# Performance work log

Measured on AMD Instinct MI355X. Metric: run time of the kernel, lower is better.

The kernel has to match this reference:

```python
import jax, jax.numpy as jnp
import numpy as np

PC = 512      # proposal_channels == conv_channels
INCH = 512    # in_channels of branch
B = 8
T = 64        # pyramid level length (feat_t) at order=0
TF = 256      # frame_level_feature length (clip_length)
KERNELS = [8, 16, 8, 4, 2, 2, 2]  # ConPoolingKernal
CLC = 498     # feature_lastclass channels (CLC + 2 == 500)
GROUPS = 32


def _gn(x, gamma, beta):
    # GroupNorm(32, C) over [B, C, L]
    Bb, C, L = x.shape
    xg = x.reshape(Bb, GROUPS, C // GROUPS, L)
    m = xg.mean(axis=(2, 3), keepdims=True)
    v = xg.var(axis=(2, 3), keepdims=True)
    xn = ((xg - m) * jax.lax.rsqrt(v + 1e-5)).reshape(Bb, C, L)
    return xn * gamma[None, :, None] + beta[None, :, None]


def _c1(x, w, b):
    # Unit1D kernel_shape=1: pointwise conv
    return jnp.einsum('bct,oc->bot', x, w) + b[None, :, None]


def _bmp(feat, segs):
    # BoundaryMaxPooling: first C/2 channels max-pooled over segs[...,0:2],
    # second C/2 over segs[...,2:4] (inclusive integer ranges, clamped).
    Bb, C, L = feat.shape
    C2 = C // 2
    pos = jnp.arange(L)
    def pool(f, s, e):
        s = jnp.clip(s, 0, L - 1)
        e = jnp.maximum(jnp.clip(e, 0, L - 1), s)
        mask = (pos[None, None, :] >= s[..., None]) & (pos[None, None, :] <= e[..., None])  # [B,T,L]
        return jnp.max(jnp.where(mask[:, None], f[:, :, None, :], -jnp.inf), axis=-1)  # [B,C2,T]
    return jnp.concatenate([pool(feat[:, :C2], segs[..., 0], segs[..., 1]),
                            pool(feat[:, C2:], segs[..., 2], segs[..., 3])], axis=1)


def _anchor_gather(feat, anc, K):
    # Vectorized per-anchor clamp/slice + nearest F.interpolate(size=K):
    # src index for output k of a slice [l, r] is l + floor(k * (r - l + 1) / K).
    Bb, C, L = feat.shape
    left = jnp.clip(anc[..., 0], 0, L)
    right = jnp.clip(anc[..., 1], 0, L)
    valid = right > left                      # empty slices -> zeros (torch branch)
    seglen = right + 1 - left
    k = jnp.arange(K)
    idx = jnp.clip(left[..., None] + (k[None, None, :] * seglen[..., None]) // K, 0, L - 1)  # [B,T,K]
    g = jax.vmap(lambda f, ix: f[:, ix])(feat, idx)   # [B,C,T,K]
    return g * valid[:, None, :, None].astype(feat.dtype)


def setup_inputs() -> dict:
    key = jax.random.key(0)
    ks = jax.random.split(key, 16)
    f32 = jnp.float32
    s = 0.02
    def w(k, shape):
        return jax.random.normal(k, shape, f32) * s
    inp = {}
    inp['feature'] = jax.random.normal(ks[0], (B, INCH, T), f32)
    inp['frame_level_feature'] = jax.random.normal(ks[1], (B, PC, TF), f32)
    inp['segments'] = jax.random.randint(ks[2], (B, T, 4), 0, T).astype(jnp.int32)
    inp['frame_segments'] = jax.random.randint(ks[3], (B, T, 4), 0, TF).astype(jnp.int32)
    inp['feature_lastclass'] = jax.random.normal(ks[4], (B, CLC, T), f32)
    inp['anchor'] = jnp.sort(jax.random.randint(ks[5], (B, T, 2), 0, T), axis=-1).astype(jnp.int32)
    inp['frame_anchor'] = jnp.sort(jax.random.randint(ks[6], (B, T, 2), 0, TF), axis=-1).astype(jnp.int32)
    inp['order'] = 0
    inp['LocResult_feature'] = jax.random.normal(ks[7], (B, 2, T), f32)
    inp['w_cur'] = w(ks[8], (PC, INCH)); inp['b_cur'] = jnp.zeros((PC,), f32)
    inp['g_cur'] = jnp.ones((PC,), f32); inp['be_cur'] = jnp.zeros((PC,), f32)
    inp['w_lr'] = w(ks[9], (2 * PC, INCH)); inp['b_lr'] = jnp.zeros((2 * PC,), f32)
    inp['g_lr'] = jnp.ones((2 * PC,), f32); inp['be_lr'] = jnp.zeros((2 * PC,), f32)
    inp['w_roi'] = w(ks[10], (PC, PC)); inp['b_roi'] = jnp.zeros((PC,), f32)
    inp['g_roi'] = jnp.ones((PC,), f32); inp['be_roi'] = jnp.zeros((PC,), f32)
    K1 = KERNELS[1]; K0 = KERNELS[0]
    inp['w_cp'] = w(ks[11], (PC, 2 * PC, K1)); inp['b_cp'] = jnp.zeros((PC,), f32)
    inp['w_cp0'] = w(ks[12], (PC, PC, K0)); inp['b_cp0'] = jnp.zeros((PC,), f32)
    CIN = 6 * PC + 500
    inp['w_prop'] = w(ks[13], (INCH, CIN)); inp['b_prop'] = jnp.zeros((INCH,), f32)
    inp['g_prop'] = jnp.ones((INCH,), f32); inp['be_prop'] = jnp.zeros((INCH,), f32)
    return inp


def reference(feature, frame_level_feature, segments, frame_segments, feature_lastclass,
              anchor, frame_anchor, order, LocResult_feature,
              w_cur, b_cur, g_cur, be_cur, w_lr, b_lr, g_lr, be_lr,
              w_roi, b_roi, g_roi, be_roi, w_cp, b_cp, w_cp0, b_cp0,
              w_prop, b_prop, g_prop, be_prop):
    relu = jax.nn.relu
    fm_short = relu(_gn(_c1(feature, w_cur, b_cur), g_cur, be_cur))           # [B,PC,T]
    feat_lr = relu(_gn(_c1(feature, w_lr, b_lr), g_lr, be_lr))                # [B,2PC,T]
    prop_feature = _bmp(feat_lr, segments)                                    # [B,2PC,T]
    prop_roi = relu(_gn(_c1(_bmp(frame_level_feature, frame_segments), w_roi, b_roi), g_roi, be_roi))
    K1 = KERNELS[order + 1]
    K0 = KERNELS[0]
    g1 = _anchor_gather(feat_lr, anchor, K1)                                  # [B,2PC,T,K1]
    con_feature = jnp.einsum('bctk,ock->bot', g1, w_cp) + b_cp[None, :, None]  # valid conv K1->1
    g0 = _anchor_gather(frame_level_feature, frame_anchor, K0)                # [B,PC,T,K0]
    frame_con = jnp.einsum('bctk,ock->bot', g0, w_cp0) + b_cp0[None, :, None]
    prop_con = relu(_gn(_c1(frame_con, w_roi, b_roi), g_roi, be_roi))
    cat = jnp.concatenate([prop_roi, prop_feature, fm_short, feature_lastclass,
                           con_feature, prop_con, LocResult_feature], axis=1)  # [B,6PC+500,T]
    out = relu(_gn(_c1(cat, w_prop, b_prop), g_prop, be_prop))                # [B,INCH,T]
    return (out, feat_lr)
```

## Files before the change

kernel.cpp:

```cpp
#include <hip/hip_runtime.h>
#include <math.h>

#define BB 8
#define CATP 3584
#define CAT_REAL 3572

typedef __attribute__((ext_vector_type(8))) short short8;
typedef __attribute__((ext_vector_type(4))) float f32x4;

__device__ inline ushort f2bf(float f) {
  union { float f; unsigned u; } x;
  x.f = f;
  return (ushort)((x.u + 0x7FFFu + ((x.u >> 16) & 1u)) >> 16);
}
__device__ inline float bf2f(unsigned us) {
  union { unsigned u; float f; } x;
  x.u = us << 16;
  return x.f;
}

__global__ __launch_bounds__(256) void cvt_wfrag_kernel(
    const float* __restrict__ w_cur, const float* __restrict__ w_lr,
    const float* __restrict__ w_roi, const float* __restrict__ w_prop,
    ushort* __restrict__ Wcomb, ushort* __restrict__ Wroi,
    ushort* __restrict__ Wprop) {
  const int i = blockIdx.x * 256 + threadIdx.x;
  const float* src;
  ushort* dst;
  int o, k8, Kc;
  bool pad = false;
  if (i < 98304) {
    o = i >> 6; k8 = i & 63; Kc = 16;
    src = (o < 512) ? (w_cur + (size_t)o * 512) : (w_lr + (size_t)(o - 512) * 512);
    dst = Wcomb;
  } else if (i < 131072) {
    const int r = i - 98304;
    o = r >> 6; k8 = r & 63; Kc = 16;
    src = w_roi + (size_t)o * 512;
    dst = Wroi;
  } else {
    const int r = i - 131072;
    if (r >= 229376) return;
    o = r / 448; k8 = r % 448; Kc = 112;
    src = w_prop + (size_t)o * CAT_REAL;
    dst = Wprop;
    pad = true;
  }
  const int k = k8 * 8;
  float v[8];
  if (pad) {
#pragma unroll
    for (int q = 0; q < 8; q++) v[q] = (k + q < CAT_REAL) ? src[k + q] : 0.f;
  } else {
    const float4 f0 = *(const float4*)(src + k);
    const float4 f1 = *(const float4*)(src + k + 4);
    v[0] = f0.x; v[1] = f0.y; v[2] = f0.z; v[3] = f0.w;
    v[4] = f1.x; v[5] = f1.y; v[6] = f1.z; v[7] = f1.w;
  }
  uint4 pk;
  pk.x = (unsigned)f2bf(v[0]) | ((unsigned)f2bf(v[1]) << 16);
  pk.y = (unsigned)f2bf(v[2]) | ((unsigned)f2bf(v[3]) << 16);
  pk.z = (unsigned)f2bf(v[4]) | ((unsigned)f2bf(v[5]) << 16);
  pk.w = (unsigned)f2bf(v[6]) | ((unsigned)f2bf(v[7]) << 16);
  const int ot = o >> 6, ii = (o >> 4) & 3, l15 = o & 15;
  const int kc = k8 >> 2, l4 = k8 & 3;
  const size_t flat =
      ((((size_t)ot * Kc + kc) * 4 + ii) * 64 + l4 * 16 + l15) * 8;
  *(uint4*)(dst + flat) = pk;
}

template <int Cin, int Kf>
__device__ void cpT_body(const float* __restrict__ W, ushort* __restrict__ D,
                         int o, float* tile ) {
  const int nt = o >> 6, j = (o >> 4) & 3, l15 = o & 15;
  for (int c0 = 0; c0 < Cin; c0 += 256) {
    __syncthreads();
    for (int e = threadIdx.x; e < 256 * Kf; e += 256) {
      const int c = e / Kf, k = e % Kf;
      tile[c * (Kf + 1) + k] = W[((size_t)o * Cin + c0) * Kf + e];
    }
    __syncthreads();
    for (int e = threadIdx.x; e < Kf * 32; e += 256) {
      const int k = e >> 5, c8 = e & 31;
      const int cl = c8 * 8;
      const int c = c0 + cl;
      uint4 pk;
      pk.x = (unsigned)f2bf(tile[(cl + 0) * (Kf + 1) + k]) |
             ((unsigned)f2bf(tile[(cl + 1) * (Kf + 1) + k]) << 16);
      pk.y = (unsigned)f2bf(tile[(cl + 2) * (Kf + 1) + k]) |
             ((unsigned)f2bf(tile[(cl + 3) * (Kf + 1) + k]) << 16);
      pk.z = (unsigned)f2bf(tile[(cl + 4) * (Kf + 1) + k]) |
             ((unsigned)f2bf(tile[(cl + 5) * (Kf + 1) + k]) << 16);
      pk.w = (unsigned)f2bf(tile[(cl + 6) * (Kf + 1) + k]) |
             ((unsigned)f2bf(tile[(cl + 7) * (Kf + 1) + k]) << 16);
      const int cc = c >> 5, l4 = (c >> 3) & 3;
      const size_t flat =
          ((((size_t)nt * Kf + k) * (Cin >> 5) + cc) * 4 + j) * 512 +
          (l4 * 16 + l15) * 8;
      *(uint4*)(D + flat) = pk;
    }
  }
}

__global__ __launch_bounds__(256) void cvt_cpT_kernel(
    const float* __restrict__ w_cp, ushort* __restrict__ WcpT,
    const float* __restrict__ w_cp0, ushort* __restrict__ Wcp0T) {
  __shared__ float tile[256 * 17];
  const int bid = blockIdx.x;
  if (bid < 512)
    cpT_body<1024, 16>(w_cp, WcpT, bid, tile);
  else
    cpT_body<512, 8>(w_cp0, Wcp0T, bid - 512, tile);
}

__global__ __launch_bounds__(256) void transpose_multi_kernel(
    const float* __restrict__ feature, const float* __restrict__ frame_feat,
    const float* __restrict__ lastcls, const float* __restrict__ locres,
    ushort* __restrict__ Ft, ushort* __restrict__ FfT,
    ushort* __restrict__ cat) {
  const int bid = blockIdx.x;
  const float* src;
  ushort* dst;
  int Cr, Cw, L, rs, co, cblk, lblk, b;
  if (bid < 64) {
    src = feature; dst = Ft; Cr = 512; Cw = 512; L = 64; rs = 512; co = 0;
    cblk = bid & 7; lblk = 0; b = bid >> 3;
  } else if (bid < 320) {
    const int r = bid - 64;
    src = frame_feat; dst = FfT; Cr = 512; Cw = 512; L = 256; rs = 512; co = 0;
    cblk = r & 7; lblk = (r >> 3) & 3; b = r >> 5;
  } else if (bid < 384) {
    const int r = bid - 320;
    src = lastcls; dst = cat; Cr = 498; Cw = 498; L = 64; rs = CATP; co = 2048;
    cblk = r & 7; lblk = 0; b = r >> 3;
  } else {
    const int r = bid - 384;
    src = locres; dst = cat; Cr = 2; Cw = 14; L = 64; rs = CATP; co = 3570;
    cblk = 0; lblk = 0; b = r;
  }
  __shared__ float tile[64 * 65];
  const int c0 = cblk * 64, l0 = lblk * 64;
  for (int e = threadIdx.x; e < 4096; e += 256) {
    const int cc = e >> 6, ll = e & 63;
    const int c = c0 + cc;
    tile[cc * 65 + ll] = (c < Cr) ? src[((size_t)b * Cr + c) * L + l0 + ll] : 0.f;
  }
  __syncthreads();
  for (int e = threadIdx.x; e < 4096; e += 256) {
    const int ll = e >> 6, cc = e & 63;
    const int c = c0 + cc;
    if (c < Cw)
      dst[((size_t)b * L + l0 + ll) * rs + co + c] = f2bf(tile[cc * 65 + ll]);
  }
}

__global__ __launch_bounds__(256) void gemm_gn_seg_kernel(
    int nblk0,
    const ushort* __restrict__ X0, const ushort* __restrict__ W0,
    const float* __restrict__ b0, const float* __restrict__ g0,
    const float* __restrict__ e0, int Kp0, int cs0, float* of0, int om0,
    ushort* co0, int cst0, int coff0,
    const ushort* __restrict__ X1, const ushort* __restrict__ W1,
    const float* __restrict__ b1, const float* __restrict__ g1,
    const float* __restrict__ e1, int Kp1, int cs1, float* of1, int om1,
    ushort* co1, int cst1, int coff1) {
  const int bx = blockIdx.x;
  const bool s1 = bx >= nblk0;
  const ushort* Xt = s1 ? X1 : X0;
  const ushort* Wb = s1 ? W1 : W0;
  const float* bias = s1 ? b1 : b0;
  const float* gamma = s1 ? g1 : g0;
  const float* beta = s1 ? e1 : e0;
  const int Kp = s1 ? Kp1 : Kp0;
  const int cpgShift = s1 ? cs1 : cs0;
  float* outF = s1 ? of1 : of0;
  const int outFM = s1 ? om1 : om0;
  ushort* catOut = s1 ? co1 : co0;
  const int catStride = s1 ? cst1 : cst0;
  const int chOff = s1 ? coff1 : coff0;
  const int o0 = (s1 ? bx - nblk0 : bx) * 64;

  const int b = blockIdx.y;
  const int w = threadIdx.x >> 6;
  const int lane = threadIdx.x & 63;
  const int l15 = lane & 15, l4 = lane >> 4;
  const int wk = Kp >> 2;
  const int kbeg = w * wk, kend = kbeg + wk;

  f32x4 acc[4][4] = {};
  const ushort* wbase = Wb + (size_t)(o0 >> 6) * (Kp >> 5) * 2048 + lane * 8;
  const ushort* bp[4];
#pragma unroll
  for (int j = 0; j < 4; j++)
    bp[j] = Xt + (size_t)(b * 64 + j * 16 + l15) * Kp + l4 * 8;

  for (int k = kbeg; k < kend; k += 32) {
    const int kc = k >> 5;
    short8 a[4], x[4];
#pragma unroll
    for (int i = 0; i < 4; i++)
      a[i] = *(const short8*)(wbase + ((size_t)kc * 4 + i) * 512);
#pragma unroll
    for (int j = 0; j < 4; j++) x[j] = *(const short8*)(bp[j] + k);
#pragma unroll
    for (int i = 0; i < 4; i++)
#pragma unroll
      for (int j = 0; j < 4; j++)
        acc[i][j] = __builtin_amdgcn_mfma_f32_16x16x32_bf16(a[i], x[j],
                                                            acc[i][j], 0, 0, 0);
  }

  __shared__ float red[64 * 65];
  for (int ww = 0; ww < 4; ww++) {
    __syncthreads();
    if (w == ww) {
#pragma unroll
      for (int i = 0; i < 4; i++)
#pragma unroll
        for (int j = 0; j < 4; j++)
#pragma unroll
          for (int r = 0; r < 4; r++) {
            const int m = i * 16 + l4 * 4 + r;
            const int n = j * 16 + l15;
            if (ww == 0)
              red[m * 65 + n] = acc[i][j][r] + bias[o0 + m];
            else
              red[m * 65 + n] += acc[i][j][r];
          }
    }
  }
  __syncthreads();

  const int cpg = 1 << cpgShift;
  const int ngroups = 64 >> cpgShift;
  __shared__ float rs[4], rss[4], gmean[4], grstd[4];
  for (int gi = 0; gi < ngroups; gi++) {
    float s = 0.f, ss = 0.f;
    const int nel = cpg << 6;
    for (int e = threadIdx.x; e < nel; e += 256) {
      const float v = red[((gi << cpgShift) + (e >> 6)) * 65 + (e & 63)];
      s += v;
      ss += v * v;
    }
#pragma unroll
    for (int off = 32; off > 0; off >>= 1) {
      s += __shfl_down(s, off);
      ss += __shfl_down(ss, off);
    }
    if (lane == 0) { rs[w] = s; rss[w] = ss; }
    __syncthreads();
    if (threadIdx.x == 0) {
      const float ts = rs[0] + rs[1] + rs[2] + rs[3];
      const float tss = rss[0] + rss[1] + rss[2] + rss[3];
      const float mean = ts / (float)nel;
      const float var = tss / (float)nel - mean * mean;
      gmean[gi] = mean;
      grstd[gi] = rsqrtf(var + 1e-5f);
    }
    __syncthreads();
  }

  if (outF) {
    for (int e = threadIdx.x; e < 4096; e += 256) {
      const int m = e >> 6, n = e & 63;
      const int gi = m >> cpgShift;
      const int c = o0 + m;
      float v = (red[m * 65 + n] - gmean[gi]) * grstd[gi] * gamma[c] + beta[c];
      v = fmaxf(v, 0.f);
      outF[((size_t)b * outFM + c) * 64 + n] = v;
    }
  }
  if (catOut) {
    for (int e = threadIdx.x; e < 4096; e += 256) {
      const int n = e >> 6, m = e & 63;
      const int gi = m >> cpgShift;
      const int c = o0 + m;
      float v = (red[m * 65 + n] - gmean[gi]) * grstd[gi] * gamma[c] + beta[c];
      v = fmaxf(v, 0.f);
      catOut[((size_t)(b * 64) + n) * catStride + chOff + c] = f2bf(v);
    }
  }
}

template <int C, int L>
__device__ void bmp_body(const ushort* __restrict__ Xt,
                         const int* __restrict__ segs, ushort* __restrict__ Y,
                         int rowStride, int chOff, float2 (*pmax)[512]) {
  constexpr int C2 = C / 2;
  constexpr int P2 = C2 / 2;
  constexpr int CH = P2 / 64;
  const int t = blockIdx.x;
  const int b = blockIdx.y;
  const int w = threadIdx.x >> 6;
  const int lane = threadIdx.x & 63;
  const int* sg = segs + ((size_t)b * 64 + t) * 4;
  const ushort* Xb = Xt + (size_t)b * L * C;
#pragma unroll
  for (int h = 0; h < 2; h++) {
    const int s = min(max(sg[2 * h], 0), L - 1);
    const int e = max(min(max(sg[2 * h + 1], 0), L - 1), s);
#pragma unroll
    for (int q = 0; q < CH; q++) {
      const int p = q * 64 + lane;
      const ushort* base = Xb + h * C2 + 2 * p;
      float a0 = -INFINITY, a1 = -INFINITY;
      float c0 = -INFINITY, c1 = -INFINITY;
      int l = s + w;
      for (; l + 4 <= e; l += 8) {
        const unsigned u0 = *(const unsigned*)(base + (size_t)l * C);
        const unsigned u1 = *(const unsigned*)(base + (size_t)(l + 4) * C);
        a0 = fmaxf(a0, bf2f(u0 & 0xffffu));
        a1 = fmaxf(a1, bf2f(u0 >> 16));
        c0 = fmaxf(c0, bf2f(u1 & 0xffffu));
        c1 = fmaxf(c1, bf2f(u1 >> 16));
      }
      if (l <= e) {
        const unsigned u0 = *(const unsigned*)(base + (size_t)l * C);
        a0 = fmaxf(a0, bf2f(u0 & 0xffffu));
        a1 = fmaxf(a1, bf2f(u0 >> 16));
      }
      pmax[w][h * P2 + p] = make_float2(fmaxf(a0, c0), fmaxf(a1, c1));
    }
  }
  __syncthreads();
  for (int idx = threadIdx.x; idx < 2 * P2; idx += 256) {
    float2 m = pmax[0][idx];
#pragma unroll
    for (int ww = 1; ww < 4; ww++) {
      const float2 v = pmax[ww][idx];
      m.x = fmaxf(m.x, v.x);
      m.y = fmaxf(m.y, v.y);
    }
    const unsigned o = (unsigned)f2bf(m.x) | ((unsigned)f2bf(m.y) << 16);
    *(unsigned*)(Y + ((size_t)(b * 64) + t) * rowStride + chOff + 2 * idx) = o;
  }
}

__global__ __launch_bounds__(256) void bmp_dual_kernel(
    const ushort* __restrict__ FlrT, const int* __restrict__ segments,
    ushort* __restrict__ cat, const ushort* __restrict__ FfT,
    const int* __restrict__ frame_segs, ushort* __restrict__ XbmpT) {
  __shared__ float2 pm[4][512];
  if (blockIdx.z == 0)
    bmp_body<1024, 64>(FlrT, segments, cat, CATP, 512, pm);
  else
    bmp_body<512, 256>(FfT, frame_segs, XbmpT, 512, 0, pm);
}

template <int Kf, int L, int Cin>
__device__ void anchor_mfma_body(const ushort* __restrict__ src,
                                 const int* __restrict__ anc,
                                 const ushort* __restrict__ Wt,
                                 float* __restrict__ P, int slice, float* red) {
  const int nt = blockIdx.x;
  const int b = blockIdx.y;
  const int w = threadIdx.x >> 6;
  const int lane = threadIdx.x & 63;
  const int l15 = lane & 15, l4 = lane >> 4;
  const int kz = slice >> 1, chalf = slice & 1;
  const int k = kz * 4 + w;
  const int cbase = chalf * (Cin / 2);

  const ushort* rp[4];
#pragma unroll
  for (int i = 0; i < 4; i++) {
    const int t = i * 16 + l15;
    const int a0 = anc[((size_t)b * 64 + t) * 2 + 0];
    const int a1 = anc[((size_t)b * 64 + t) * 2 + 1];
    const int left = min(max(a0, 0), L);
    const int right = min(max(a1, 0), L);
    const int seglen = right + 1 - left;
    const int ix = min(max(left + (k * seglen) / Kf, 0), L - 1);
    rp[i] = src + ((size_t)b * L + ix) * Cin + cbase + l4 * 8;
  }
  const ushort* wb = Wt + (size_t)(nt * Kf + k) * (Cin >> 5) * 2048 + lane * 8;

  f32x4 acc[4][4] = {};
  for (int c0 = 0; c0 < Cin / 2; c0 += 32) {
    const int cc = (cbase + c0) >> 5;
    short8 a[4], bb[4];
#pragma unroll
    for (int i = 0; i < 4; i++) a[i] = *(const short8*)(rp[i] + c0);
#pragma unroll
    for (int j = 0; j < 4; j++)
      bb[j] = *(const short8*)(wb + ((size_t)cc * 4 + j) * 512);
#pragma unroll
    for (int i = 0; i < 4; i++)
#pragma unroll
      for (int j = 0; j < 4; j++)
        acc[i][j] = __builtin_amdgcn_mfma_f32_16x16x32_bf16(a[i], bb[j],
                                                            acc[i][j], 0, 0, 0);
  }

  for (int ww = 0; ww < 4; ww++) {
    __syncthreads();
    if (w == ww) {
#pragma unroll
      for (int i = 0; i < 4; i++)
#pragma unroll
        for (int j = 0; j < 4; j++)
#pragma unroll
          for (int r = 0; r < 4; r++) {
            const int m = i * 16 + l4 * 4 + r;
            const int n = j * 16 + l15;
            if (ww == 0)
              red[m * 65 + n] = acc[i][j][r];
            else
              red[m * 65 + n] += acc[i][j][r];
          }
    }
  }
  __syncthreads();
  float* Pp = P + (((size_t)slice * BB + b) * 512 + nt * 64) * 64;
  for (int e = threadIdx.x; e < 4096; e += 256) {
    const int n = e >> 6, m = e & 63;
    Pp[e] = red[m * 65 + n];
  }
}

__global__ __launch_bounds__(256) void anchor_mfma_dual_kernel(
    const ushort* __restrict__ FlrT, const int* __restrict__ anchor,
    const ushort* __restrict__ WcpT, float* __restrict__ P1,
    const ushort* __restrict__ FfT, const int* __restrict__ frame_anchor,
    const ushort* __restrict__ Wcp0T, float* __restrict__ P0) {
  __shared__ float red[64 * 65];
  const int z = blockIdx.z;
  if (z < 8)
    anchor_mfma_body<16, 64, 1024>(FlrT, anchor, WcpT, P1, z, red);
  else
    anchor_mfma_body<8, 256, 512>(FfT, frame_anchor, Wcp0T, P0, z - 8, red);
}

__device__ void anchor_reduce_body(const float* __restrict__ P, int ks,
                                   const float* __restrict__ bias,
                                   const int* __restrict__ anc, int L,
                                   ushort* __restrict__ Y, int rowStride,
                                   int chOff, float* tile, float* sval) {
  const int o0 = blockIdx.x * 64;
  const int b = blockIdx.y;
  if (threadIdx.x < 64) {
    const int t = threadIdx.x;
    const int a0 = anc[((size_t)b * 64 + t) * 2 + 0];
    const int a1 = anc[((size_t)b * 64 + t) * 2 + 1];
    const int left = min(max(a0, 0), L);
    const int right = min(max(a1, 0), L);
    sval[t] = (right > left) ? 1.f : 0.f;
  }
  __syncthreads();
  for (int e = threadIdx.x; e < 4096; e += 256) {
    const int nl = e >> 6, m = e & 63;
    const int n = o0 + nl;
    float s = 0.f;
    for (int z = 0; z < ks; z++)
      s += P[(((size_t)z * BB + b) * 512 + n) * 64 + m];
    tile[nl * 65 + m] = s * sval[m] + bias[n];
  }
  __syncthreads();
  for (int e = threadIdx.x; e < 4096; e += 256) {
    const int m = e >> 6, nl = e & 63;
    Y[((size_t)(b * 64) + m) * rowStride + chOff + o0 + nl] =
        f2bf(tile[nl * 65 + m]);
  }
}

__global__ __launch_bounds__(256) void anchor_reduce_dual_kernel(
    const float* __restrict__ P1, const float* __restrict__ b_cp,
    const int* __restrict__ anchor, ushort* __restrict__ cat,
    const float* __restrict__ P0, const float* __restrict__ b_cp0,
    const int* __restrict__ frame_anchor, ushort* __restrict__ FconT) {
  __shared__ float tile[64 * 65];
  __shared__ float sval[64];
  if (blockIdx.z == 0)
    anchor_reduce_body(P1, 8, b_cp, anchor, 64, cat, CATP, 2546, tile, sval);
  else
    anchor_reduce_body(P0, 4, b_cp0, frame_anchor, 256, FconT, 512, 0, tile, sval);
}

extern "C" void kernel_launch(void* const* d_in, const int* in_sizes, int n_in,
                              void* d_out, int out_size, void* d_ws,
                              size_t ws_size, hipStream_t stream) {
  const float* feature      = (const float*)d_in[0];
  const float* frame_feat   = (const float*)d_in[1];
  const int*   segments     = (const int*)d_in[2];
  const int*   frame_segs   = (const int*)d_in[3];
  const float* feat_lastcls = (const float*)d_in[4];
  const int*   anchor       = (const int*)d_in[5];
  const int*   frame_anchor = (const int*)d_in[6];
  const float* locres       = (const float*)d_in[8];
  const float* w_cur  = (const float*)d_in[9];
  const float* b_cur  = (const float*)d_in[10];
  const float* g_cur  = (const float*)d_in[11];
  const float* be_cur = (const float*)d_in[12];
  const float* w_lr   = (const float*)d_in[13];
  const float* b_lr   = (const float*)d_in[14];
  const float* g_lr   = (const float*)d_in[15];
  const float* be_lr  = (const float*)d_in[16];
  const float* w_roi  = (const float*)d_in[17];
  const float* b_roi  = (const float*)d_in[18];
  const float* g_roi  = (const float*)d_in[19];
  const float* be_roi = (const float*)d_in[20];
  const float* w_cp   = (const float*)d_in[21];
  const float* b_cp   = (const float*)d_in[22];
  const float* w_cp0  = (const float*)d_in[23];
  const float* b_cp0  = (const float*)d_in[24];
  const float* w_prop = (const float*)d_in[25];
  const float* b_prop = (const float*)d_in[26];
  const float* g_prop = (const float*)d_in[27];
  const float* be_prop= (const float*)d_in[28];

  float* out_main = (float*)d_out;
  float* feat_lr  = (float*)d_out + BB * 512 * 64;

  ushort* cat_t  = (ushort*)d_ws;
  ushort* Ft     = cat_t + 1835008;
  ushort* XbmpT  = Ft + 262144;
  ushort* FconT  = XbmpT + 262144;
  ushort* Wcomb  = FconT + 262144;
  ushort* Wroi   = Wcomb + 786432;
  ushort* Wprop  = Wroi + 262144;
  ushort* WcpT   = Wprop + 1835008;
  ushort* Wcp0T  = WcpT + 8388608;
  ushort* FlrT   = Wcp0T + 2097152;
  ushort* FfT    = FlrT + 524288;
  float*  P1     = (float*)(FfT + 1048576);
  float*  P0     = P1 + 2097152;

  cvt_wfrag_kernel<<<1408, 256, 0, stream>>>(
      w_cur, w_lr, w_roi, w_prop, Wcomb, Wroi, Wprop);

  cvt_cpT_kernel<<<1024, 256, 0, stream>>>(w_cp, WcpT, w_cp0, Wcp0T);

  transpose_multi_kernel<<<392, 256, 0, stream>>>(
      feature, frame_feat, feat_lastcls, locres, Ft, FfT, cat_t);

  gemm_gn_seg_kernel<<<dim3(24, BB), 256, 0, stream>>>(
      8,
      Ft, Wcomb, b_cur, g_cur, be_cur, 512, 4, nullptr, 0, cat_t, CATP, 1536,
      Ft, Wcomb + 512 * 512, b_lr, g_lr, be_lr, 512, 5, feat_lr, 1024, FlrT,
      1024, 0);

  bmp_dual_kernel<<<dim3(64, BB, 2), 256, 0, stream>>>(
      FlrT, segments, cat_t, FfT, frame_segs, XbmpT);

  anchor_mfma_dual_kernel<<<dim3(8, BB, 12), 256, 0, stream>>>(
      FlrT, anchor, WcpT, P1, FfT, frame_anchor, Wcp0T, P0);

  anchor_reduce_dual_kernel<<<dim3(8, BB, 2), 256, 0, stream>>>(
      P1, b_cp, anchor, cat_t, P0, b_cp0, frame_anchor, FconT);

  gemm_gn_seg_kernel<<<dim3(16, BB), 256, 0, stream>>>(
      8,
      XbmpT, Wroi, b_roi, g_roi, be_roi, 512, 4, nullptr, 0, cat_t, CATP, 0,
      FconT, Wroi, b_roi, g_roi, be_roi, 512, 4, nullptr, 0, cat_t, CATP, 3058);

  gemm_gn_seg_kernel<<<dim3(8, BB), 256, 0, stream>>>(
      8,
      cat_t, Wprop, b_prop, g_prop, be_prop, CATP, 4, out_main, 512, nullptr,
      CATP, 0,
      cat_t, Wprop, b_prop, g_prop, be_prop, CATP, 4, nullptr, 0, nullptr,
      CATP, 0);
}
```

Baseline: 308.6 us.

## Fuse prep kernels, register-transpose conv weights, split-K final GEMM with reduce

Merges the three weight/feature conversion kernels into one prep launch, which removes two launches. The conv-pool weight transpose now runs in registers with float4 loads, with no shared-memory tile or barriers. The final 3584-wide GEMM, which previously ran on only 64 blocks, is split across 4 K-chunks into fp32 partials. A separate kernel then reduces the partials and applies bias, GroupNorm and ReLU. This raises parallelism for the largest GEMM, at the cost of extra partial-buffer traffic and one more launch.

```diff
diff --git a/kernel.cpp b/kernel.cpp
--- a/kernel.cpp
+++ b/kernel.cpp
@@ -19,126 +19,126 @@
   return x.f;
 }
 
-__global__ __launch_bounds__(256) void cvt_wfrag_kernel(
+template <int Cin, int Kf>
+__device__ void cpT_tile(const float* __restrict__ W, ushort* __restrict__ D,
+                         int nt, int cc) {
+  const int tid = threadIdx.x;
+  const int j = tid >> 6, l4 = (tid >> 4) & 3, l15 = tid & 15;
+  const int o = nt * 64 + j * 16 + l15;
+  const int cb = cc * 32 + l4 * 8;
+  ushort rg[8][Kf];
+#pragma unroll
+  for (int q = 0; q < 8; q++) {
+    const float* row = W + ((size_t)o * Cin + cb + q) * Kf;
+#pragma unroll
+    for (int kq = 0; kq < Kf / 4; kq++) {
+      const float4 f = *(const float4*)(row + kq * 4);
+      rg[q][kq * 4 + 0] = f2bf(f.x);
+      rg[q][kq * 4 + 1] = f2bf(f.y);
+      rg[q][kq * 4 + 2] = f2bf(f.z);
+      rg[q][kq * 4 + 3] = f2bf(f.w);
+    }
+  }
+#pragma unroll
+  for (int k = 0; k < Kf; k++) {
+    uint4 pk;
+    pk.x = (unsigned)rg[0][k] | ((unsigned)rg[1][k] << 16);
+    pk.y = (unsigned)rg[2][k] | ((unsigned)rg[3][k] << 16);
+    pk.z = (unsigned)rg[4][k] | ((unsigned)rg[5][k] << 16);
+    pk.w = (unsigned)rg[6][k] | ((unsigned)rg[7][k] << 16);
+    *(uint4*)(D + ((size_t)(nt * Kf + k) * (Cin >> 5) + cc) * 2048 + tid * 8) = pk;
+  }
+}
+
+__global__ __launch_bounds__(256) void prep_kernel(
     const float* __restrict__ w_cur, const float* __restrict__ w_lr,
     const float* __restrict__ w_roi, const float* __restrict__ w_prop,
     ushort* __restrict__ Wcomb, ushort* __restrict__ Wroi,
-    ushort* __restrict__ Wprop) {
-  const int i = blockIdx.x * 256 + threadIdx.x;
-  const float* src;
-  ushort* dst;
-  int o, k8, Kc;
-  bool pad = false;
-  if (i < 98304) {
-    o = i >> 6; k8 = i & 63; Kc = 16;
-    src = (o < 512) ? (w_cur + (size_t)o * 512) : (w_lr + (size_t)(o - 512) * 512);
-    dst = Wcomb;
-  } else if (i < 131072) {
-    const int r = i - 98304;
-    o = r >> 6; k8 = r & 63; Kc = 16;
-    src = w_roi + (size_t)o * 512;
-    dst = Wroi;
-  } else {
-    const int r = i - 131072;
-    if (r >= 229376) return;
-    o = r / 448; k8 = r % 448; Kc = 112;
-    src = w_prop + (size_t)o * CAT_REAL;
-    dst = Wprop;
-    pad = true;
-  }
-  const int k = k8 * 8;
-  float v[8];
-  if (pad) {
-#pragma unroll
-    for (int q = 0; q < 8; q++) v[q] = (k + q < CAT_REAL) ? src[k + q] : 0.f;
-  } else {
-    const float4 f0 = *(const float4*)(src + k);
-    const float4 f1 = *(const float4*)(src + k + 4);
-    v[0] = f0.x; v[1] = f0.y; v[2] = f0.z; v[3] = f0.w;
-    v[4] = f1.x; v[5] = f1.y; v[6] = f1.z; v[7] = f1.w;
-  }
-  uint4 pk;
-  pk.x = (unsigned)f2bf(v[0]) | ((unsigned)f2bf(v[1]) << 16);
-  pk.y = (unsigned)f2bf(v[2]) | ((unsigned)f2bf(v[3]) << 16);
-  pk.z = (unsigned)f2bf(v[4]) | ((unsigned)f2bf(v[5]) << 16);
-  pk.w = (unsigned)f2bf(v[6]) | ((unsigned)f2bf(v[7]) << 16);
-  const int ot = o >> 6, ii = (o >> 4) & 3, l15 = o & 15;
-  const int kc = k8 >> 2, l4 = k8 & 3;
-  const size_t flat =
-      ((((size_t)ot * Kc + kc) * 4 + ii) * 64 + l4 * 16 + l15) * 8;
-  *(uint4*)(dst + flat) = pk;
-}
-
-template <int Cin, int Kf>
-__device__ void cpT_body(const float* __restrict__ W, ushort* __restrict__ D,
-                         int o, float* tile ) {
-  const int nt = o >> 6, j = (o >> 4) & 3, l15 = o & 15;
-  for (int c0 = 0; c0 < Cin; c0 += 256) {
-    __syncthreads();
-    for (int e = threadIdx.x; e < 256 * Kf; e += 256) {
-      const int c = e / Kf, k = e % Kf;
-      tile[c * (Kf + 1) + k] = W[((size_t)o * Cin + c0) * Kf + e];
-    }
-    __syncthreads();
-    for (int e = threadIdx.x; e < Kf * 32; e += 256) {
-      const int k = e >> 5, c8 = e & 31;
-      const int cl = c8 * 8;
-      const int c = c0 + cl;
-      uint4 pk;
-      pk.x = (unsigned)f2bf(tile[(cl + 0) * (Kf + 1) + k]) |
-             ((unsigned)f2bf(tile[(cl + 1) * (Kf + 1) + k]) << 16);
-      pk.y = (unsigned)f2bf(tile[(cl + 2) * (Kf + 1) + k]) |
-             ((unsigned)f2bf(tile[(cl + 3) * (Kf + 1) + k]) << 16);
-      pk.z = (unsigned)f2bf(tile[(cl + 4) * (Kf + 1) + k]) |
-             ((unsigned)f2bf(tile[(cl + 5) * (Kf + 1) + k]) << 16);
-      pk.w = (unsigned)f2bf(tile[(cl + 6) * (Kf + 1) + k]) |
-             ((unsigned)f2bf(tile[(cl + 7) * (Kf + 1) + k]) << 16);
-      const int cc = c >> 5, l4 = (c >> 3) & 3;
-      const size_t flat =
-          ((((size_t)nt * Kf + k) * (Cin >> 5) + cc) * 4 + j) * 512 +
-          (l4 * 16 + l15) * 8;
-      *(uint4*)(D + flat) = pk;
-    }
-  }
-}
-
-__global__ __launch_bounds__(256) void cvt_cpT_kernel(
-    const float* __restrict__ w_cp, ushort* __restrict__ WcpT,
-    const float* __restrict__ w_cp0, ushort* __restrict__ Wcp0T) {
-  __shared__ float tile[256 * 17];
+    ushort* __restrict__ Wprop, const float* __restrict__ w_cp,
+    ushort* __restrict__ WcpT, const float* __restrict__ w_cp0,
+    ushort* __restrict__ Wcp0T, const float* __restrict__ feature,
+    const float* __restrict__ frame_feat, const float* __restrict__ lastcls,
+    const float* __restrict__ locres, ushort* __restrict__ Ft,
+    ushort* __restrict__ FfT, ushort* __restrict__ cat) {
+  __shared__ float tile[64 * 65];
   const int bid = blockIdx.x;
-  if (bid < 512)
-    cpT_body<1024, 16>(w_cp, WcpT, bid, tile);
-  else
-    cpT_body<512, 8>(w_cp0, Wcp0T, bid - 512, tile);
-}
-
-__global__ __launch_bounds__(256) void transpose_multi_kernel(
-    const float* __restrict__ feature, const float* __restrict__ frame_feat,
-    const float* __restrict__ lastcls, const float* __restrict__ locres,
-    ushort* __restrict__ Ft, ushort* __restrict__ FfT,
-    ushort* __restrict__ cat) {
-  const int bid = blockIdx.x;
+  if (bid < 1408) {
+    const int i = bid * 256 + threadIdx.x;
+    const float* src;
+    ushort* dst;
+    int o, k8, Kc;
+    bool pad = false;
+    if (i < 98304) {
+      o = i >> 6; k8 = i & 63; Kc = 16;
+      src = (o < 512) ? (w_cur + (size_t)o * 512)
+                      : (w_lr + (size_t)(o - 512) * 512);
+      dst = Wcomb;
+    } else if (i < 131072) {
+      const int r = i - 98304;
+      o = r >> 6; k8 = r & 63; Kc = 16;
+      src = w_roi + (size_t)o * 512;
+      dst = Wroi;
+    } else {
+      const int r = i - 131072;
+      if (r >= 229376) return;
+      o = r / 448; k8 = r % 448; Kc = 112;
+      src = w_prop + (size_t)o * CAT_REAL;
+      dst = Wprop;
+      pad = true;
+    }
+    const int k = k8 * 8;
+    float v[8];
+    if (pad) {
+#pragma unroll
+      for (int q = 0; q < 8; q++) v[q] = (k + q < CAT_REAL) ? src[k + q] : 0.f;
+    } else {
+      const float4 f0 = *(const float4*)(src + k);
+      const float4 f1 = *(const float4*)(src + k + 4);
+      v[0] = f0.x; v[1] = f0.y; v[2] = f0.z; v[3] = f0.w;
+      v[4] = f1.x; v[5] = f1.y; v[6] = f1.z; v[7] = f1.w;
+    }
+    uint4 pk;
+    pk.x = (unsigned)f2bf(v[0]) | ((unsigned)f2bf(v[1]) << 16);
+    pk.y = (unsigned)f2bf(v[2]) | ((unsigned)f2bf(v[3]) << 16);
+    pk.z = (unsigned)f2bf(v[4]) | ((unsigned)f2bf(v[5]) << 16);
+    pk.w = (unsigned)f2bf(v[6]) | ((unsigned)f2bf(v[7]) << 16);
+    const int ot = o >> 6, ii = (o >> 4) & 3, l15 = o & 15;
+    const int kc = k8 >> 2, l4 = k8 & 3;
+    const size_t flat =
+        ((((size_t)ot * Kc + kc) * 4 + ii) * 64 + l4 * 16 + l15) * 8;
+    *(uint4*)(dst + flat) = pk;
+    return;
+  }
+  if (bid < 1792) {
+    const int local = bid - 1408;
+    if (local < 256)
+      cpT_tile<1024, 16>(w_cp, WcpT, local >> 5, local & 31);
+    else {
+      const int r = local - 256;
+      cpT_tile<512, 8>(w_cp0, Wcp0T, r >> 4, r & 15);
+    }
+    return;
+  }
+  const int local = bid - 1792;
   const float* src;
   ushort* dst;
   int Cr, Cw, L, rs, co, cblk, lblk, b;
-  if (bid < 64) {
+  if (local < 64) {
     src = feature; dst = Ft; Cr = 512; Cw = 512; L = 64; rs = 512; co = 0;
-    cblk = bid & 7; lblk = 0; b = bid >> 3;
-  } else if (bid < 320) {
-    const int r = bid - 64;
+    cblk = local & 7; lblk = 0; b = local >> 3;
+  } else if (local < 320) {
+    const int r = local - 64;
     src = frame_feat; dst = FfT; Cr = 512; Cw = 512; L = 256; rs = 512; co = 0;
     cblk = r & 7; lblk = (r >> 3) & 3; b = r >> 5;
-  } else if (bid < 384) {
-    const int r = bid - 320;
+  } else if (local < 384) {
+    const int r = local - 320;
     src = lastcls; dst = cat; Cr = 498; Cw = 498; L = 64; rs = CATP; co = 2048;
     cblk = r & 7; lblk = 0; b = r >> 3;
   } else {
-    const int r = bid - 384;
+    const int r = local - 384;
     src = locres; dst = cat; Cr = 2; Cw = 14; L = 64; rs = CATP; co = 3570;
     cblk = 0; lblk = 0; b = r;
   }
-  __shared__ float tile[64 * 65];
   const int c0 = cblk * 64, l0 = lblk * 64;
   for (int e = threadIdx.x; e < 4096; e += 256) {
     const int cc = e >> 6, ll = e & 63;
@@ -279,6 +279,118 @@
       v = fmaxf(v, 0.f);
       catOut[((size_t)(b * 64) + n) * catStride + chOff + c] = f2bf(v);
     }
+  }
+}
+
+__global__ __launch_bounds__(256) void gemm_part_kernel(
+    const ushort* __restrict__ Xt, const ushort* __restrict__ Wb,
+    float* __restrict__ P) {
+  const int ot = blockIdx.x;
+  const int b = blockIdx.y;
+  const int kz = blockIdx.z;
+  const int w = threadIdx.x >> 6;
+  const int lane = threadIdx.x & 63;
+  const int l15 = lane & 15, l4 = lane >> 4;
+  const int kbeg = kz * 896 + w * 224;
+  const int kend = kbeg + 224;
+
+  f32x4 acc[4][4] = {};
+  const ushort* wbase = Wb + (size_t)ot * (CATP >> 5) * 2048 + lane * 8;
+  const ushort* bp[4];
+#pragma unroll
+  for (int j = 0; j < 4; j++)
+    bp[j] = Xt + (size_t)(b * 64 + j * 16 + l15) * CATP + l4 * 8;
+
+  for (int k = kbeg; k < kend; k += 32) {
+    const int kc = k >> 5;
+    short8 a[4], x[4];
+#pragma unroll
+    for (int i = 0; i < 4; i++)
+      a[i] = *(const short8*)(wbase + ((size_t)kc * 4 + i) * 512);
+#pragma unroll
+    for (int j = 0; j < 4; j++) x[j] = *(const short8*)(bp[j] + k);
+#pragma unroll
+    for (int i = 0; i < 4; i++)
+#pragma unroll
+      for (int j = 0; j < 4; j++)
+        acc[i][j] = __builtin_amdgcn_mfma_f32_16x16x32_bf16(a[i], x[j],
+                                                            acc[i][j], 0, 0, 0);
+  }
+
+  __shared__ float red[64 * 65];
+  for (int ww = 0; ww < 4; ww++) {
+    __syncthreads();
+    if (w == ww) {
+#pragma unroll
+      for (int i = 0; i < 4; i++)
+#pragma unroll
+        for (int j = 0; j < 4; j++)
+#pragma unroll
+          for (int r = 0; r < 4; r++) {
+            const int m = i * 16 + l4 * 4 + r;
+            const int n = j * 16 + l15;
+            if (ww == 0)
+              red[m * 65 + n] = acc[i][j][r];
+            else
+              red[m * 65 + n] += acc[i][j][r];
+          }
+    }
+  }
+  __syncthreads();
+  float* Pp = P + (((size_t)kz * BB + b) * 512 + ot * 64) * 64;
+  for (int e = threadIdx.x; e < 4096; e += 256) Pp[e] = red[(e >> 6) * 65 + (e & 63)];
+}
+
+__global__ __launch_bounds__(256) void reduce_gn_kernel(
+    const float* __restrict__ P, const float* __restrict__ bias,
+    const float* __restrict__ gamma, const float* __restrict__ beta,
+    float* __restrict__ outF) {
+  const int ot = blockIdx.x;
+  const int b = blockIdx.y;
+  const int o0 = ot * 64;
+  const int w = threadIdx.x >> 6;
+  const int lane = threadIdx.x & 63;
+  __shared__ float red[64 * 65];
+  for (int e = threadIdx.x; e < 4096; e += 256) {
+    const int m = e >> 6, n = e & 63;
+    float s = bias[o0 + m];
+#pragma unroll
+    for (int z = 0; z < 4; z++)
+      s += P[(((size_t)z * BB + b) * 512 + o0 + m) * 64 + n];
+    red[m * 65 + n] = s;
+  }
+  __syncthreads();
+  __shared__ float rs[4], rss[4], gmean[4], grstd[4];
+  for (int gi = 0; gi < 4; gi++) {
+    float s = 0.f, ss = 0.f;
+    for (int e = threadIdx.x; e < 1024; e += 256) {
+      const float v = red[((gi << 4) + (e >> 6)) * 65 + (e & 63)];
+      s += v;
+      ss += v * v;
+    }
+#pragma unroll
+    for (int off = 32; off > 0; off >>= 1) {
+      s += __shfl_down(s, off);
+      ss += __shfl_down(ss, off);
+    }
+    if (lane == 0) { rs[w] = s; rss[w] = ss; }
+    __syncthreads();
+    if (threadIdx.x == 0) {
+      const float ts = rs[0] + rs[1] + rs[2] + rs[3];
+      const float tss = rss[0] + rss[1] + rss[2] + rss[3];
+      const float mean = ts / 1024.f;
+      const float var = tss / 1024.f - mean * mean;
+      gmean[gi] = mean;
+      grstd[gi] = rsqrtf(var + 1e-5f);
+    }
+    __syncthreads();
+  }
+  for (int e = threadIdx.x; e < 4096; e += 256) {
+    const int m = e >> 6, n = e & 63;
+    const int gi = m >> 4;
+    const int c = o0 + m;
+    float v = (red[m * 65 + n] - gmean[gi]) * grstd[gi] * gamma[c] + beta[c];
+    outF[((size_t)b * 512 + c) * 64 + n] = fmaxf(v, 0.f);
   }
 }
 
@@ -524,14 +636,11 @@
   ushort* FfT    = FlrT + 524288;
   float*  P1     = (float*)(FfT + 1048576);
   float*  P0     = P1 + 2097152;
-
-  cvt_wfrag_kernel<<<1408, 256, 0, stream>>>(
-      w_cur, w_lr, w_roi, w_prop, Wcomb, Wroi, Wprop);
-
-  cvt_cpT_kernel<<<1024, 256, 0, stream>>>(w_cp, WcpT, w_cp0, Wcp0T);
-
-  transpose_multi_kernel<<<392, 256, 0, stream>>>(
-      feature, frame_feat, feat_lastcls, locres, Ft, FfT, cat_t);
+  float*  P9     = P0 + 1048576;
+
+  prep_kernel<<<2184, 256, 0, stream>>>(
+      w_cur, w_lr, w_roi, w_prop, Wcomb, Wroi, Wprop, w_cp, WcpT, w_cp0,
+      Wcp0T, feature, frame_feat, feat_lastcls, locres, Ft, FfT, cat_t);
 
   gemm_gn_seg_kernel<<<dim3(24, BB), 256, 0, stream>>>(
       8,
@@ -553,10 +662,8 @@
       XbmpT, Wroi, b_roi, g_roi, be_roi, 512, 4, nullptr, 0, cat_t, CATP, 0,
       FconT, Wroi, b_roi, g_roi, be_roi, 512, 4, nullptr, 0, cat_t, CATP, 3058);
 
-  gemm_gn_seg_kernel<<<dim3(8, BB), 256, 0, stream>>>(
-      8,
-      cat_t, Wprop, b_prop, g_prop, be_prop, CATP, 4, out_main, 512, nullptr,
-      CATP, 0,
-      cat_t, Wprop, b_prop, g_prop, be_prop, CATP, 4, nullptr, 0, nullptr,
-      CATP, 0);
-}
+  gemm_part_kernel<<<dim3(8, BB, 4), 256, 0, stream>>>(cat_t, Wprop, P9);
+
+  reduce_gn_kernel<<<dim3(8, BB), 256, 0, stream>>>(
+      P9, b_prop, g_prop, be_prop, out_main);
+}
```

New measurement: 266.7 us. -13.6%, faster.
